# Optimization experiments

Measured on AMD Instinct MI355X. Metric: run time of the kernel, lower is better.

The kernel has to match this reference:

```python
import jax, jax.numpy as jnp
import numpy as np
from jax import lax

B, N, C = 8, 8192, 64
ODR, K, OUT = 4, 32, 128
S = N // ODR
EPS = 1e-5


def _lbr(h, W, b, g, be):
    # h: [M, K, Cin] -> linear -> BN (training-mode batch stats over (M,K) per channel) -> relu
    y = jnp.einsum('mki,oi->mko', h, W) + b
    mean = y.mean(axis=(0, 1))
    var = ((y - mean) ** 2).mean(axis=(0, 1))  # biased var, as torch BN uses for normalization
    y = (y - mean) * lax.rsqrt(var + EPS) * g + be
    return jax.nn.relu(y)


def setup_inputs() -> dict:
    key = jax.random.key(0)
    ks = jax.random.split(key, 12)
    x = jax.random.normal(ks[0], (B, N, C), dtype=jnp.float32)
    coor = jax.random.normal(ks[1], (B, N, 3), dtype=jnp.float32)
    indx = jax.random.permutation(ks[2], N)[:S]  # like torch.randperm(N)[:S]
    w1 = jax.random.normal(ks[3], (OUT, 2 * C), dtype=jnp.float32) * (2 * C) ** -0.5
    b1 = jax.random.normal(ks[4], (OUT,), dtype=jnp.float32) * 0.01
    g1 = jax.random.uniform(ks[5], (OUT,), dtype=jnp.float32, minval=0.5, maxval=1.5)
    be1 = jax.random.normal(ks[6], (OUT,), dtype=jnp.float32) * 0.01
    w2 = jax.random.normal(ks[7], (OUT, OUT), dtype=jnp.float32) * OUT ** -0.5
    b2 = jax.random.normal(ks[8], (OUT,), dtype=jnp.float32) * 0.01
    g2 = jax.random.uniform(ks[9], (OUT,), dtype=jnp.float32, minval=0.5, maxval=1.5)
    be2 = jax.random.normal(ks[10], (OUT,), dtype=jnp.float32) * 0.01
    return dict(x=x, coor=coor, indx=indx, w1=w1, b1=b1, g1=g1, be1=be1,
                w2=w2, b2=b2, g2=g2, be2=be2)


def reference(x, coor, indx, w1, b1, g1, be1, w2, b2, g2, be2):
    sampled_coor = coor[:, indx, :]  # [B,S,3]
    sampled_x = x[:, indx, :]        # [B,S,C]
    # pairwise squared distances [B,S,N]
    dist = jnp.sum((coor[:, None, :, :] - sampled_coor[:, :, None, :]) ** 2, axis=-1)
    # k smallest distances == argsort(dist)[..., :K]
    _, knn_idx = lax.top_k(-dist, K)  # [B,S,K]
    knn_x = jax.vmap(lambda xb, ib: xb[ib])(x, knn_idx)  # [B,S,K,C]
    rep_x = jnp.broadcast_to(sampled_x[:, :, None, :], (x.shape[0], S, K, x.shape[2]))
    feat = jnp.concatenate([rep_x, knn_x - rep_x], axis=-1)  # [B,S,K,2C]
    feat = feat.reshape(x.shape[0] * S, K, 2 * x.shape[2])
    h = _lbr(feat, w1, b1, g1, be1)
    h = _lbr(h, w2, b2, g2, be2)
    h = h.reshape(x.shape[0], S, K, -1)
    out = jnp.max(h, axis=2)  # [B,S,OUT]
    return out, sampled_coor
```

## Files before the change

### kernel.cpp

```cpp
#include <hip/hip_runtime.h>
#include <stdint.h>


#define N_    8192
#define GPB_  16

typedef __attribute__((ext_vector_type(8))) short bf8;
typedef __attribute__((ext_vector_type(16))) float f32x16;
typedef __attribute__((ext_vector_type(2))) float f32x2;

__device__ __forceinline__ unsigned int bf1u(float f) {
  unsigned int u = __float_as_uint(f);
  return (u + 0x7fffu + ((u >> 16) & 1u)) >> 16;
}
__device__ __forceinline__ unsigned int bfpair(float lo, float hi) {
  return bf1u(lo) | (bf1u(hi) << 16);
}

__device__ __forceinline__ f32x2 pk_add(f32x2 a, f32x2 b) {
  f32x2 d;
  asm("v_pk_add_f32 %0, %1, %2" : "=v"(d) : "v"(a), "v"(b));
  return d;
}
__device__ __forceinline__ f32x2 pk_mul(f32x2 a, f32x2 b) {
  f32x2 d;
  asm("v_pk_mul_f32 %0, %1, %2" : "=v"(d) : "v"(a), "v"(b));
  return d;
}

__global__ __launch_bounds__(256) void kprep(const float* __restrict__ w1,
                                             const float* __restrict__ w2,
                                             const float* __restrict__ coor,
                                             const int* __restrict__ indx,
                                             unsigned short* __restrict__ w1b,
                                             unsigned short* __restrict__ w2b,
                                             float* __restrict__ outc,
                                             float* __restrict__ soa) {
  int e = blockIdx.x * 256 + threadIdx.x;
  if (e < 16384) {
    w1b[e] = (unsigned short)bf1u(w1[e]);
  } else if (e < 32768) {
    int e2 = e - 16384;
    w2b[e2] = (unsigned short)bf1u(w2[e2]);
  } else if (e < 81920) {
    int e2 = e - 32768;
    int bs = e2 / 3, c = e2 - bs * 3;
    int b = bs >> 11, s = bs & 2047;
    outc[e2] = coor[(b * N_ + indx[s]) * 3 + c];
  } else {
    int p = e - 81920;
    const int b = p >> 13, i = p & 8191;
    const float* src = coor + (size_t)p * 3;
    float* dst = soa + b * 24576;
    dst[i]         = src[0];
    dst[8192 + i]  = src[1];
    dst[16384 + i] = src[2];
  }
}

__global__ __launch_bounds__(256, 8) void kknn(const float* __restrict__ soa,
                                               const int* __restrict__ indx,
                                               int* __restrict__ knn) {
  __shared__ __align__(16) float4 sdist4[4 * 256];
  __shared__ float sTw[8];
  __shared__ unsigned long long cands[192];
  __shared__ int ccnt;

  const int gid = blockIdx.x;
  const int b = gid >> 11, s = gid & 2047;
  const int tid = threadIdx.x;
  const int w = tid >> 6, lane = tid & 63;
  const int hl = lane & 31;
  const float* Xb = soa + b * 24576;
  const float* Yb = Xb + 8192;
  const float* Zb = Xb + 16384;
  const int qi = indx[s];
  const float qx = Xb[qi], qy = Yb[qi], qz = Zb[qi];
  const f32x2 nqx = {-qx, -qx}, nqy = {-qy, -qy}, nqz = {-qz, -qz};

  f32x2 rd[8];
  float dmA = 3.4e38f, dmB = 3.4e38f;
#pragma unroll
  for (int it = 0; it < 8; ++it) {
    const int ofs = (it << 10) + (tid << 2);
    union { float4 f4; f32x2 h[2]; } X, Y, Z;
    X.f4 = *(const float4*)(Xb + ofs);
    Y.f4 = *(const float4*)(Yb + ofs);
    Z.f4 = *(const float4*)(Zb + ofs);
    const f32x2 dxl = pk_add(X.h[0], nqx), dyl = pk_add(Y.h[0], nqy),
                dzl = pk_add(Z.h[0], nqz);
    const f32x2 dxh = pk_add(X.h[1], nqx), dyh = pk_add(Y.h[1], nqy),
                dzh = pk_add(Z.h[1], nqz);
    const f32x2 sl =
        pk_add(pk_add(pk_mul(dxl, dxl), pk_mul(dyl, dyl)), pk_mul(dzl, dzl));
    const f32x2 sh =
        pk_add(pk_add(pk_mul(dxh, dxh), pk_mul(dyh, dyh)), pk_mul(dzh, dzh));
    dmA = fminf(fminf(sl.x, sl.y), dmA);
    dmB = fminf(fminf(sh.x, sh.y), dmB);
    if (it < 4) {
      rd[it * 2] = sl;
      rd[it * 2 + 1] = sh;
    } else {
      union { float4 f4; f32x2 h[2]; } st;
      st.h[0] = sl;
      st.h[1] = sh;
      sdist4[((it - 4) << 8) + tid] = st.f4;
    }
  }
  float dmin = fminf(dmA, dmB);
  if (tid == 0) ccnt = 0;
  if (tid < 192) cands[tid] = ~0ULL;

  float v = dmin;
#pragma unroll
  for (int k = 2; k <= 32; k <<= 1) {
#pragma unroll
    for (int j = k >> 1; j >= 1; j >>= 1) {
      const float o = __shfl_xor(v, j, 64);
      const bool dirAsc = ((hl & k) == 0);
      const bool lower = ((hl & j) == 0);
      const float lo = fminf(v, o), hi = fmaxf(v, o);
      v = (dirAsc == lower) ? lo : hi;
    }
  }
  if (hl == 3) sTw[(w << 1) + (lane >> 5)] = v;
  __syncthreads();
  const float T =
      fmaxf(fmaxf(fmaxf(sTw[0], sTw[1]), fmaxf(sTw[2], sTw[3])),
            fmaxf(fmaxf(sTw[4], sTw[5]), fmaxf(sTw[6], sTw[7])));

#pragma unroll
  for (int t = 0; t < 8; ++t) {
    const int p0 = ((t >> 1) << 10) + (tid << 2) + ((t & 1) << 1);
    const float d0 = rd[t].x, d1 = rd[t].y;
    if (d0 <= T) {
      const int pos = atomicAdd(&ccnt, 1);
      if (pos < 192)
        cands[pos] = ((unsigned long long)__float_as_uint(d0) << 32) |
                     (unsigned int)p0;
    }
    if (d1 <= T) {
      const int pos = atomicAdd(&ccnt, 1);
      if (pos < 192)
        cands[pos] = ((unsigned long long)__float_as_uint(d1) << 32) |
                     (unsigned int)(p0 + 1);
    }
  }
#pragma unroll
  for (int it = 4; it < 8; ++it) {
    const float4 d4 = sdist4[((it - 4) << 8) + tid];
    const int p0 = (it << 10) + (tid << 2);
    const float dd[4] = {d4.x, d4.y, d4.z, d4.w};
#pragma unroll
    for (int j = 0; j < 4; ++j) {
      if (dd[j] <= T) {
        const int pos = atomicAdd(&ccnt, 1);
        if (pos < 192)
          cands[pos] = ((unsigned long long)__float_as_uint(dd[j]) << 32) |
                       (unsigned int)(p0 + j);
      }
    }
  }
  __syncthreads();

  const int E = min(ccnt, 192);
  if (tid < E) {
    const unsigned long long key = cands[tid];
    int rank = 0;
    const int Ep = (E + 3) & ~3;
#pragma unroll 4
    for (int j = 0; j < Ep; ++j) rank += (cands[j] < key) ? 1 : 0;
    if (rank < 32) knn[gid * 32 + rank] = (int)(unsigned int)key;
  }
}

template <int PHASE>
__global__ __launch_bounds__(256, 2) void kphase(
    const float* __restrict__ x, const int* __restrict__ indx,
    const int* __restrict__ knn, const float* __restrict__ b1,
    const unsigned short* __restrict__ w1b, const unsigned short* __restrict__ w2b,
    const float* __restrict__ b2, const float* __restrict__ st1,
    float* __restrict__ part, float* __restrict__ mout) {
  __shared__ __align__(16) unsigned short sxb[4][80];
  __shared__ __align__(16) unsigned short dls[4][32 * 68 + 8];
  __shared__ __align__(16) unsigned short h1[PHASE == 2 ? 2 * 32 * 136 : 8];

  const int tid = threadIdx.x;
  const int w = tid >> 6;
  const int lane = tid & 63;
  const int m = lane & 31, q2 = lane >> 5;
  const int col = (w << 5) + m;
  const int r8 = tid >> 3, c8 = (tid & 7) * 8;

  const int bb = blockIdx.x & 7;
  const int jj = blockIdx.x >> 3;
  const float* xb = x + (size_t)bb * (N_ * 64);
  const int gidbase = (bb << 11) + jj * GPB_;
  const int sbase = jj * GPB_;

  bf8 bf1[8];
#pragma unroll
  for (int t = 0; t < 8; ++t)
    bf1[t] = *(const bf8*)&w1b[col * 128 + t * 16 + q2 * 8];
  bf8 bf2[8];
  float s1 = 0.f, t1 = 0.f, b2v = 0.f;
  if constexpr (PHASE == 2) {
#pragma unroll
    for (int t = 0; t < 8; ++t)
      bf2[t] = *(const bf8*)&w2b[col * 128 + t * 16 + q2 * 8];
    s1 = st1[col];
    t1 = st1[128 + col];
    b2v = b2[col];
  }
  (void)w2b; (void)b2; (void)st1; (void)mout;
  const float b1c = b1[col];

  float sum = 0.f, ssq = 0.f;

  float4 caA, ccA, gaA, gcA, caB, ccB, gaB, gcB;
  {
    const int idxA = indx[sbase];
    const int idxB = indx[sbase + 1];
    const int nbrA = knn[(size_t)gidbase * 32 + r8];
    const int nbrB = knn[(size_t)(gidbase + 1) * 32 + r8];
    const float* cA = xb + (size_t)idxA * 64;
    caA = *(const float4*)(cA + c8);
    ccA = *(const float4*)(cA + c8 + 4);
    const float* gA = xb + (size_t)nbrA * 64;
    gaA = *(const float4*)(gA + c8);
    gcA = *(const float4*)(gA + c8 + 4);
    const float* cB = xb + (size_t)idxB * 64;
    caB = *(const float4*)(cB + c8);
    ccB = *(const float4*)(cB + c8 + 4);
    const float* gB = xb + (size_t)nbrB * 64;
    gaB = *(const float4*)(gB + c8);
    gcB = *(const float4*)(gB + c8 + 4);
  }
  int idxA2 = (GPB_ > 2) ? indx[sbase + 2] : 0;
  int idxB2 = (GPB_ > 3) ? indx[sbase + 3] : 0;
  int nbrA2 = (GPB_ > 2) ? knn[(size_t)(gidbase + 2) * 32 + r8] : 0;
  int nbrB2 = (GPB_ > 3) ? knn[(size_t)(gidbase + 3) * 32 + r8] : 0;

#pragma unroll 1
  for (int g = 0; g < GPB_; g += 2) {
    const int gid = gidbase + g;
    const int p0 = g & 3, p1 = (g + 1) & 3;

    float4 caA_n = caA, ccA_n = ccA, gaA_n = gaA, gcA_n = gcA;
    float4 caB_n = caB, ccB_n = ccB, gaB_n = gaB, gcB_n = gcB;
    if (g + 2 < GPB_) {
      const float* cA = xb + (size_t)idxA2 * 64;
      caA_n = *(const float4*)(cA + c8);
      ccA_n = *(const float4*)(cA + c8 + 4);
      const float* gA = xb + (size_t)nbrA2 * 64;
      gaA_n = *(const float4*)(gA + c8);
      gcA_n = *(const float4*)(gA + c8 + 4);
      const float* cB = xb + (size_t)idxB2 * 64;
      caB_n = *(const float4*)(cB + c8);
      ccB_n = *(const float4*)(cB + c8 + 4);
      const float* gB = xb + (size_t)nbrB2 * 64;
      gaB_n = *(const float4*)(gB + c8);
      gcB_n = *(const float4*)(gB + c8 + 4);
    }
    if (g + 4 < GPB_) {
      nbrA2 = knn[(size_t)(gid + 4) * 32 + r8];
      nbrB2 = knn[(size_t)(gid + 5) * 32 + r8];
      idxA2 = indx[sbase + g + 4];
      idxB2 = indx[sbase + g + 5];
    }

    {
      uint2 lo, hi;
      lo.x = bfpair(gaA.x - caA.x, gaA.y - caA.y);
      lo.y = bfpair(gaA.z - caA.z, gaA.w - caA.w);
      hi.x = bfpair(gcA.x - ccA.x, gcA.y - ccA.y);
      hi.y = bfpair(gcA.z - ccA.z, gcA.w - ccA.w);
      *(uint2*)&dls[p0][r8 * 68 + c8] = lo;
      *(uint2*)&dls[p0][r8 * 68 + c8 + 4] = hi;
      lo.x = bfpair(gaB.x - caB.x, gaB.y - caB.y);
      lo.y = bfpair(gaB.z - caB.z, gaB.w - caB.w);
      hi.x = bfpair(gcB.x - ccB.x, gcB.y - ccB.y);
      hi.y = bfpair(gcB.z - ccB.z, gcB.w - ccB.w);
      *(uint2*)&dls[p1][r8 * 68 + c8] = lo;
      *(uint2*)&dls[p1][r8 * 68 + c8 + 4] = hi;
    }
    if (tid < 8) {
      uint2 lo, hi;
      lo.x = bfpair(caA.x, caA.y);
      lo.y = bfpair(caA.z, caA.w);
      hi.x = bfpair(ccA.x, ccA.y);
      hi.y = bfpair(ccA.z, ccA.w);
      *(uint2*)&sxb[p0][tid * 8] = lo;
      *(uint2*)&sxb[p0][tid * 8 + 4] = hi;
      lo.x = bfpair(caB.x, caB.y);
      lo.y = bfpair(caB.z, caB.w);
      hi.x = bfpair(ccB.x, ccB.y);
      hi.y = bfpair(ccB.z, ccB.w);
      *(uint2*)&sxb[p1][tid * 8] = lo;
      *(uint2*)&sxb[p1][tid * 8 + 4] = hi;
    }
    asm volatile("s_waitcnt lgkmcnt(0)" ::: "memory");
    __builtin_amdgcn_s_barrier();

#pragma unroll
    for (int mem = 0; mem < 2; ++mem) {
      const int pb = mem == 0 ? p0 : p1;
      bf8 af[8];
#pragma unroll
      for (int t = 0; t < 4; ++t) {
        union { bf8 v; uint2 u[2]; } fa;
        fa.u[0] = *(const uint2*)&sxb[pb][t * 16 + q2 * 8];
        fa.u[1] = *(const uint2*)&sxb[pb][t * 16 + q2 * 8 + 4];
        af[t] = fa.v;
      }
#pragma unroll
      for (int t = 0; t < 4; ++t) {
        union { bf8 v; uint2 u[2]; } fa;
        fa.u[0] = *(const uint2*)&dls[pb][m * 68 + t * 16 + q2 * 8];
        fa.u[1] = *(const uint2*)&dls[pb][m * 68 + t * 16 + q2 * 8 + 4];
        af[4 + t] = fa.v;
      }
      f32x16 acc;
#pragma unroll
      for (int r = 0; r < 16; ++r) acc[r] = b1c;
#pragma unroll
      for (int t = 0; t < 8; ++t)
        acc = __builtin_amdgcn_mfma_f32_32x32x16_bf16(af[t], bf1[t], acc, 0, 0, 0);

      if constexpr (PHASE == 1) {
#pragma unroll
        for (int r = 0; r < 16; ++r) {
          const float v = acc[r];
          sum += v;
          ssq = fmaf(v, v, ssq);
        }
      } else {
        const int hp = mem * (32 * 136);
#pragma unroll
        for (int r = 0; r < 16; ++r) {
          const float hv = fmaxf(0.f, fmaf(acc[r], s1, t1));
          const int row = (r & 3) + ((r >> 2) << 3) + (q2 << 2);
          h1[hp + row * 136 + col] = (unsigned short)bf1u(hv);
        }
      }
    }

    if constexpr (PHASE == 2) {
      asm volatile("s_waitcnt lgkmcnt(0)" ::: "memory");
      __builtin_amdgcn_s_barrier();
#pragma unroll
      for (int mem = 0; mem < 2; ++mem) {
        const int hp = mem * (32 * 136);
        f32x16 acc2;
#pragma unroll
        for (int r = 0; r < 16; ++r) acc2[r] = b2v;
#pragma unroll
        for (int t = 0; t < 8; ++t) {
          const bf8 a2 = *(const bf8*)&h1[hp + m * 136 + t * 16 + q2 * 8];
          acc2 = __builtin_amdgcn_mfma_f32_32x32x16_bf16(a2, bf2[t], acc2, 0, 0, 0);
        }
        float mx = -1e30f;
#pragma unroll
        for (int r = 0; r < 16; ++r) {
          const float v = acc2[r];
          sum += v;
          ssq = fmaf(v, v, ssq);
          mx = fmaxf(mx, v);
        }
        mx = fmaxf(mx, __shfl_xor(mx, 32, 64));
        if (lane < 32) mout[(size_t)(gid + mem) * 128 + col] = mx;
      }
    }

    caA = caA_n; ccA = ccA_n; gaA = gaA_n; gcA = gcA_n;
    caB = caB_n; ccB = ccB_n; gaB = gaB_n; gcB = gcB_n;
  }

  sum += __shfl_xor(sum, 32, 64);
  ssq += __shfl_xor(ssq, 32, 64);
  if (lane < 32) {
    part[blockIdx.x * 256 + col] = sum;
    part[blockIdx.x * 256 + 128 + col] = ssq;
  }
}

__global__ __launch_bounds__(256) void kred1(const float* __restrict__ part,
                                             double* __restrict__ dbuf) {
  const int blk = blockIdx.x;
  const int c = threadIdx.x;
  const float* p = part + (size_t)blk * 16 * 256 + c;
  double acc = 0.0;
#pragma unroll
  for (int r = 0; r < 16; ++r) acc += (double)p[r * 256];
  dbuf[blk * 256 + c] = acc;
}

__global__ __launch_bounds__(256) void kred2(const double* __restrict__ dbuf,
                                             const float* __restrict__ gam,
                                             const float* __restrict__ bet,
                                             float* __restrict__ st) {
  __shared__ double sS[256];
  const int c = threadIdx.x;
  double acc = 0.0;
#pragma unroll 8
  for (int i = 0; i < 64; ++i) acc += dbuf[i * 256 + c];
  sS[c] = acc;
  __syncthreads();
  if (c < 128) {
    const double Sv = sS[c], SSv = sS[128 + c];
    const double cnt = 524288.0;
    const double mean = Sv / cnt;
    const double var = SSv / cnt - mean * mean;
    const double scale = (double)gam[c] / sqrt(var + 1e-5);
    st[c] = (float)scale;
    st[128 + c] = (float)((double)bet[c] - mean * scale);
  }
}

__global__ __launch_bounds__(256) void kout(const float* __restrict__ m,
                                            const float* __restrict__ st2,
                                            float* __restrict__ out) {
  const int e4 = blockIdx.x * 256 + threadIdx.x;
  const int o0 = (e4 & 31) * 4;
  const float4 v = ((const float4*)m)[e4];
  const float4 sc = *(const float4*)&st2[o0];
  const float4 sh = *(const float4*)&st2[128 + o0];
  float4 r;
  r.x = fmaxf(0.f, fmaf(v.x, sc.x, sh.x));
  r.y = fmaxf(0.f, fmaf(v.y, sc.y, sh.y));
  r.z = fmaxf(0.f, fmaf(v.z, sc.z, sh.z));
  r.w = fmaxf(0.f, fmaf(v.w, sc.w, sh.w));
  ((float4*)out)[e4] = r;
}

extern "C" void kernel_launch(void* const* d_in, const int* in_sizes, int n_in,
                              void* d_out, int out_size, void* d_ws, size_t ws_size,
                              hipStream_t stream) {
  (void)in_sizes; (void)n_in; (void)out_size; (void)ws_size;
  const float* x    = (const float*)d_in[0];
  const float* coor = (const float*)d_in[1];
  const int*   indx = (const int*)d_in[2];
  const float* w1   = (const float*)d_in[3];
  const float* b1   = (const float*)d_in[4];
  const float* g1   = (const float*)d_in[5];
  const float* be1  = (const float*)d_in[6];
  const float* w2   = (const float*)d_in[7];
  const float* b2   = (const float*)d_in[8];
  const float* g2   = (const float*)d_in[9];
  const float* be2  = (const float*)d_in[10];
  float* out = (float*)d_out;

  char* ws = (char*)d_ws;
  int*            knn   = (int*)(ws + 0);
  float*          mbuf  = (float*)(ws + 2097152);
  float*          part1 = (float*)(ws + 10485760);
  float*          soa   = (float*)(ws + 10485760);
  float*          part2 = (float*)(ws + 12582912);
  unsigned short* w1b   = (unsigned short*)(ws + 14680064);
  unsigned short* w2b   = (unsigned short*)(ws + 14712832);
  float*          st1   = (float*)(ws + 14745600);
  float*          st2   = (float*)(ws + 14746624);
  double*         dbuf  = (double*)(ws + 14747648);

  float* outc = out + 2097152;

  kprep<<<576, 256, 0, stream>>>(w1, w2, coor, indx, w1b, w2b, outc, soa);
  kknn<<<16384, 256, 0, stream>>>(soa, indx, knn);
  kphase<1><<<1024, 256, 0, stream>>>(x, indx, knn, b1, w1b, w2b, b2, nullptr,
                                      part1, nullptr);
  kred1<<<64, 256, 0, stream>>>(part1, dbuf);
  kred2<<<1, 256, 0, stream>>>(dbuf, g1, be1, st1);
  kphase<2><<<1024, 256, 0, stream>>>(x, indx, knn, b1, w1b, w2b, b2, st1,
                                      part2, mbuf);
  kred1<<<64, 256, 0, stream>>>(part2, dbuf);
  kred2<<<1, 256, 0, stream>>>(dbuf, g2, be2, st2);
  kout<<<2048, 256, 0, stream>>>(mbuf, st2, out);
}
```

Measured before the change: 243.4 us.

## Stage bf16 difference tiles in workspace during phase 1 for reuse in phase 2

```diff
diff --git a/kernel.cpp b/kernel.cpp
--- a/kernel.cpp
+++ b/kernel.cpp
@@ -4,6 +4,9 @@
 
 #define N_    8192
 #define GPB_  16
+#define TILE_OFF_  14878720ull
+#define SXB_OFF_   81987584ull
+#define WS_NEED_   84084736ull
 
 typedef __attribute__((ext_vector_type(8))) short bf8;
 typedef __attribute__((ext_vector_type(16))) float f32x16;
@@ -174,13 +177,14 @@
   }
 }
 
-template <int PHASE>
+template <int PHASE, int STAGED>
 __global__ __launch_bounds__(256, 2) void kphase(
     const float* __restrict__ x, const int* __restrict__ indx,
     const int* __restrict__ knn, const float* __restrict__ b1,
     const unsigned short* __restrict__ w1b, const unsigned short* __restrict__ w2b,
     const float* __restrict__ b2, const float* __restrict__ st1,
-    float* __restrict__ part, float* __restrict__ mout) {
+    float* __restrict__ part, float* __restrict__ mout,
+    uint4* __restrict__ tbuf, uint4* __restrict__ sbuf) {
   __shared__ __align__(16) unsigned short sxb[4][80];
   __shared__ __align__(16) unsigned short dls[4][32 * 68 + 8];
   __shared__ __align__(16) unsigned short h1[PHASE == 2 ? 2 * 32 * 136 : 8];
@@ -212,129 +216,72 @@
     t1 = st1[128 + col];
     b2v = b2[col];
   }
-  (void)w2b; (void)b2; (void)st1; (void)mout;
+  (void)w2b; (void)b2; (void)st1; (void)mout; (void)tbuf; (void)sbuf;
   const float b1c = b1[col];
 
   float sum = 0.f, ssq = 0.f;
 
-  float4 caA, ccA, gaA, gcA, caB, ccB, gaB, gcB;
-  {
-    const int idxA = indx[sbase];
-    const int idxB = indx[sbase + 1];
-    const int nbrA = knn[(size_t)gidbase * 32 + r8];
-    const int nbrB = knn[(size_t)(gidbase + 1) * 32 + r8];
-    const float* cA = xb + (size_t)idxA * 64;
-    caA = *(const float4*)(cA + c8);
-    ccA = *(const float4*)(cA + c8 + 4);
-    const float* gA = xb + (size_t)nbrA * 64;
-    gaA = *(const float4*)(gA + c8);
-    gcA = *(const float4*)(gA + c8 + 4);
-    const float* cB = xb + (size_t)idxB * 64;
-    caB = *(const float4*)(cB + c8);
-    ccB = *(const float4*)(cB + c8 + 4);
-    const float* gB = xb + (size_t)nbrB * 64;
-    gaB = *(const float4*)(gB + c8);
-    gcB = *(const float4*)(gB + c8 + 4);
-  }
-  int idxA2 = (GPB_ > 2) ? indx[sbase + 2] : 0;
-  int idxB2 = (GPB_ > 3) ? indx[sbase + 3] : 0;
-  int nbrA2 = (GPB_ > 2) ? knn[(size_t)(gidbase + 2) * 32 + r8] : 0;
-  int nbrB2 = (GPB_ > 3) ? knn[(size_t)(gidbase + 3) * 32 + r8] : 0;
+  if constexpr (PHASE == 2 && STAGED == 1) {
+    uint4 tA = tbuf[(size_t)gidbase * 256 + tid];
+    uint4 tB = tbuf[(size_t)(gidbase + 1) * 256 + tid];
+    uint4 sA, sB;
+    if (tid < 8) {
+      sA = sbuf[(size_t)gidbase * 8 + tid];
+      sB = sbuf[(size_t)(gidbase + 1) * 8 + tid];
+    }
 
 #pragma unroll 1
-  for (int g = 0; g < GPB_; g += 2) {
-    const int gid = gidbase + g;
-    const int p0 = g & 3, p1 = (g + 1) & 3;
-
-    float4 caA_n = caA, ccA_n = ccA, gaA_n = gaA, gcA_n = gcA;
-    float4 caB_n = caB, ccB_n = ccB, gaB_n = gaB, gcB_n = gcB;
-    if (g + 2 < GPB_) {
-      const float* cA = xb + (size_t)idxA2 * 64;
-      caA_n = *(const float4*)(cA + c8);
-      ccA_n = *(const float4*)(cA + c8 + 4);
-      const float* gA = xb + (size_t)nbrA2 * 64;
-      gaA_n = *(const float4*)(gA + c8);
-      gcA_n = *(const float4*)(gA + c8 + 4);
-      const float* cB = xb + (size_t)idxB2 * 64;
-      caB_n = *(const float4*)(cB + c8);
-      ccB_n = *(const float4*)(cB + c8 + 4);
-      const float* gB = xb + (size_t)nbrB2 * 64;
-      gaB_n = *(const float4*)(gB + c8);
-      gcB_n = *(const float4*)(gB + c8 + 4);
-    }
-    if (g + 4 < GPB_) {
-      nbrA2 = knn[(size_t)(gid + 4) * 32 + r8];
-      nbrB2 = knn[(size_t)(gid + 5) * 32 + r8];
-      idxA2 = indx[sbase + g + 4];
-      idxB2 = indx[sbase + g + 5];
-    }
-
-    {
-      uint2 lo, hi;
-      lo.x = bfpair(gaA.x - caA.x, gaA.y - caA.y);
-      lo.y = bfpair(gaA.z - caA.z, gaA.w - caA.w);
-      hi.x = bfpair(gcA.x - ccA.x, gcA.y - ccA.y);
-      hi.y = bfpair(gcA.z - ccA.z, gcA.w - ccA.w);
-      *(uint2*)&dls[p0][r8 * 68 + c8] = lo;
-      *(uint2*)&dls[p0][r8 * 68 + c8 + 4] = hi;
-      lo.x = bfpair(gaB.x - caB.x, gaB.y - caB.y);
-      lo.y = bfpair(gaB.z - caB.z, gaB.w - caB.w);
-      hi.x = bfpair(gcB.x - ccB.x, gcB.y - ccB.y);
-      hi.y = bfpair(gcB.z - ccB.z, gcB.w - ccB.w);
-      *(uint2*)&dls[p1][r8 * 68 + c8] = lo;
-      *(uint2*)&dls[p1][r8 * 68 + c8 + 4] = hi;
-    }
-    if (tid < 8) {
-      uint2 lo, hi;
-      lo.x = bfpair(caA.x, caA.y);
-      lo.y = bfpair(caA.z, caA.w);
-      hi.x = bfpair(ccA.x, ccA.y);
-      hi.y = bfpair(ccA.z, ccA.w);
-      *(uint2*)&sxb[p0][tid * 8] = lo;
-      *(uint2*)&sxb[p0][tid * 8 + 4] = hi;
-      lo.x = bfpair(caB.x, caB.y);
-      lo.y = bfpair(caB.z, caB.w);
-      hi.x = bfpair(ccB.x, ccB.y);
-      hi.y = bfpair(ccB.z, ccB.w);
-      *(uint2*)&sxb[p1][tid * 8] = lo;
-      *(uint2*)&sxb[p1][tid * 8 + 4] = hi;
-    }
-    asm volatile("s_waitcnt lgkmcnt(0)" ::: "memory");
-    __builtin_amdgcn_s_barrier();
-
-#pragma unroll
-    for (int mem = 0; mem < 2; ++mem) {
-      const int pb = mem == 0 ? p0 : p1;
-      bf8 af[8];
-#pragma unroll
-      for (int t = 0; t < 4; ++t) {
-        union { bf8 v; uint2 u[2]; } fa;
-        fa.u[0] = *(const uint2*)&sxb[pb][t * 16 + q2 * 8];
-        fa.u[1] = *(const uint2*)&sxb[pb][t * 16 + q2 * 8 + 4];
-        af[t] = fa.v;
-      }
-#pragma unroll
-      for (int t = 0; t < 4; ++t) {
-        union { bf8 v; uint2 u[2]; } fa;
-        fa.u[0] = *(const uint2*)&dls[pb][m * 68 + t * 16 + q2 * 8];
-        fa.u[1] = *(const uint2*)&dls[pb][m * 68 + t * 16 + q2 * 8 + 4];
-        af[4 + t] = fa.v;
-      }
-      f32x16 acc;
-#pragma unroll
-      for (int r = 0; r < 16; ++r) acc[r] = b1c;
-#pragma unroll
-      for (int t = 0; t < 8; ++t)
-        acc = __builtin_amdgcn_mfma_f32_32x32x16_bf16(af[t], bf1[t], acc, 0, 0, 0);
-
-      if constexpr (PHASE == 1) {
-#pragma unroll
-        for (int r = 0; r < 16; ++r) {
-          const float v = acc[r];
-          sum += v;
-          ssq = fmaf(v, v, ssq);
-        }
-      } else {
+    for (int g = 0; g < GPB_; g += 2) {
+      const int gid = gidbase + g;
+      const int p0 = g & 3, p1 = (g + 1) & 3;
+
+      uint4 tA_n = tA, tB_n = tB, sA_n = sA, sB_n = sB;
+      if (g + 2 < GPB_) {
+        tA_n = tbuf[(size_t)(gid + 2) * 256 + tid];
+        tB_n = tbuf[(size_t)(gid + 3) * 256 + tid];
+        if (tid < 8) {
+          sA_n = sbuf[(size_t)(gid + 2) * 8 + tid];
+          sB_n = sbuf[(size_t)(gid + 3) * 8 + tid];
+        }
+      }
+
+      *(uint2*)&dls[p0][r8 * 68 + c8] = make_uint2(tA.x, tA.y);
+      *(uint2*)&dls[p0][r8 * 68 + c8 + 4] = make_uint2(tA.z, tA.w);
+      *(uint2*)&dls[p1][r8 * 68 + c8] = make_uint2(tB.x, tB.y);
+      *(uint2*)&dls[p1][r8 * 68 + c8 + 4] = make_uint2(tB.z, tB.w);
+      if (tid < 8) {
+        *(uint2*)&sxb[p0][tid * 8] = make_uint2(sA.x, sA.y);
+        *(uint2*)&sxb[p0][tid * 8 + 4] = make_uint2(sA.z, sA.w);
+        *(uint2*)&sxb[p1][tid * 8] = make_uint2(sB.x, sB.y);
+        *(uint2*)&sxb[p1][tid * 8 + 4] = make_uint2(sB.z, sB.w);
+      }
+      asm volatile("s_waitcnt lgkmcnt(0)" ::: "memory");
+      __builtin_amdgcn_s_barrier();
+
+#pragma unroll
+      for (int mem = 0; mem < 2; ++mem) {
+        const int pb = mem == 0 ? p0 : p1;
+        bf8 af[8];
+#pragma unroll
+        for (int t = 0; t < 4; ++t) {
+          union { bf8 v; uint2 u[2]; } fa;
+          fa.u[0] = *(const uint2*)&sxb[pb][t * 16 + q2 * 8];
+          fa.u[1] = *(const uint2*)&sxb[pb][t * 16 + q2 * 8 + 4];
+          af[t] = fa.v;
+        }
+#pragma unroll
+        for (int t = 0; t < 4; ++t) {
+          union { bf8 v; uint2 u[2]; } fa;
+          fa.u[0] = *(const uint2*)&dls[pb][m * 68 + t * 16 + q2 * 8];
+          fa.u[1] = *(const uint2*)&dls[pb][m * 68 + t * 16 + q2 * 8 + 4];
+          af[4 + t] = fa.v;
+        }
+        f32x16 acc;
+#pragma unroll
+        for (int r = 0; r < 16; ++r) acc[r] = b1c;
+#pragma unroll
+        for (int t = 0; t < 8; ++t)
+          acc = __builtin_amdgcn_mfma_f32_32x32x16_bf16(af[t], bf1[t], acc, 0, 0, 0);
         const int hp = mem * (32 * 136);
 #pragma unroll
         for (int r = 0; r < 16; ++r) {
@@ -343,9 +290,7 @@
           h1[hp + row * 136 + col] = (unsigned short)bf1u(hv);
         }
       }
-    }
-
-    if constexpr (PHASE == 2) {
+
       asm volatile("s_waitcnt lgkmcnt(0)" ::: "memory");
       __builtin_amdgcn_s_barrier();
 #pragma unroll
@@ -370,10 +315,176 @@
         mx = fmaxf(mx, __shfl_xor(mx, 32, 64));
         if (lane < 32) mout[(size_t)(gid + mem) * 128 + col] = mx;
       }
-    }
-
-    caA = caA_n; ccA = ccA_n; gaA = gaA_n; gcA = gcA_n;
-    caB = caB_n; ccB = ccB_n; gaB = gaB_n; gcB = gcB_n;
+
+      tA = tA_n; tB = tB_n; sA = sA_n; sB = sB_n;
+    }
+  } else {
+    float4 caA, ccA, gaA, gcA, caB, ccB, gaB, gcB;
+    {
+      const int idxA = indx[sbase];
+      const int idxB = indx[sbase + 1];
+      const int nbrA = knn[(size_t)gidbase * 32 + r8];
+      const int nbrB = knn[(size_t)(gidbase + 1) * 32 + r8];
+      const float* cA = xb + (size_t)idxA * 64;
+      caA = *(const float4*)(cA + c8);
+      ccA = *(const float4*)(cA + c8 + 4);
+      const float* gA = xb + (size_t)nbrA * 64;
+      gaA = *(const float4*)(gA + c8);
+      gcA = *(const float4*)(gA + c8 + 4);
+      const float* cB = xb + (size_t)idxB * 64;
+      caB = *(const float4*)(cB + c8);
+      ccB = *(const float4*)(cB + c8 + 4);
+      const float* gB = xb + (size_t)nbrB * 64;
+      gaB = *(const float4*)(gB + c8);
+      gcB = *(const float4*)(gB + c8 + 4);
+    }
+    int idxA2 = (GPB_ > 2) ? indx[sbase + 2] : 0;
+    int idxB2 = (GPB_ > 3) ? indx[sbase + 3] : 0;
+    int nbrA2 = (GPB_ > 2) ? knn[(size_t)(gidbase + 2) * 32 + r8] : 0;
+    int nbrB2 = (GPB_ > 3) ? knn[(size_t)(gidbase + 3) * 32 + r8] : 0;
+
+#pragma unroll 1
+    for (int g = 0; g < GPB_; g += 2) {
+      const int gid = gidbase + g;
+      const int p0 = g & 3, p1 = (g + 1) & 3;
+
+      float4 caA_n = caA, ccA_n = ccA, gaA_n = gaA, gcA_n = gcA;
+      float4 caB_n = caB, ccB_n = ccB, gaB_n = gaB, gcB_n = gcB;
+      if (g + 2 < GPB_) {
+        const float* cA = xb + (size_t)idxA2 * 64;
+        caA_n = *(const float4*)(cA + c8);
+        ccA_n = *(const float4*)(cA + c8 + 4);
+        const float* gA = xb + (size_t)nbrA2 * 64;
+        gaA_n = *(const float4*)(gA + c8);
+        gcA_n = *(const float4*)(gA + c8 + 4);
+        const float* cB = xb + (size_t)idxB2 * 64;
+        caB_n = *(const float4*)(cB + c8);
+        ccB_n = *(const float4*)(cB + c8 + 4);
+        const float* gB = xb + (size_t)nbrB2 * 64;
+        gaB_n = *(const float4*)(gB + c8);
+        gcB_n = *(const float4*)(gB + c8 + 4);
+      }
+      if (g + 4 < GPB_) {
+        nbrA2 = knn[(size_t)(gid + 4) * 32 + r8];
+        nbrB2 = knn[(size_t)(gid + 5) * 32 + r8];
+        idxA2 = indx[sbase + g + 4];
+        idxB2 = indx[sbase + g + 5];
+      }
+
+      {
+        uint2 lo, hi;
+        lo.x = bfpair(gaA.x - caA.x, gaA.y - caA.y);
+        lo.y = bfpair(gaA.z - caA.z, gaA.w - caA.w);
+        hi.x = bfpair(gcA.x - ccA.x, gcA.y - ccA.y);
+        hi.y = bfpair(gcA.z - ccA.z, gcA.w - ccA.w);
+        *(uint2*)&dls[p0][r8 * 68 + c8] = lo;
+        *(uint2*)&dls[p0][r8 * 68 + c8 + 4] = hi;
+        if constexpr (PHASE == 1 && STAGED == 1)
+          tbuf[(size_t)gid * 256 + tid] = make_uint4(lo.x, lo.y, hi.x, hi.y);
+        lo.x = bfpair(gaB.x - caB.x, gaB.y - caB.y);
+        lo.y = bfpair(gaB.z - caB.z, gaB.w - caB.w);
+        hi.x = bfpair(gcB.x - ccB.x, gcB.y - ccB.y);
+        hi.y = bfpair(gcB.z - ccB.z, gcB.w - ccB.w);
+        *(uint2*)&dls[p1][r8 * 68 + c8] = lo;
+        *(uint2*)&dls[p1][r8 * 68 + c8 + 4] = hi;
+        if constexpr (PHASE == 1 && STAGED == 1)
+          tbuf[(size_t)(gid + 1) * 256 + tid] = make_uint4(lo.x, lo.y, hi.x, hi.y);
+      }
+      if (tid < 8) {
+        uint2 lo, hi;
+        lo.x = bfpair(caA.x, caA.y);
+        lo.y = bfpair(caA.z, caA.w);
+        hi.x = bfpair(ccA.x, ccA.y);
+        hi.y = bfpair(ccA.z, ccA.w);
+        *(uint2*)&sxb[p0][tid * 8] = lo;
+        *(uint2*)&sxb[p0][tid * 8 + 4] = hi;
+        if constexpr (PHASE == 1 && STAGED == 1)
+          sbuf[(size_t)gid * 8 + tid] = make_uint4(lo.x, lo.y, hi.x, hi.y);
+        lo.x = bfpair(caB.x, caB.y);
+        lo.y = bfpair(caB.z, caB.w);
+        hi.x = bfpair(ccB.x, ccB.y);
+        hi.y = bfpair(ccB.z, ccB.w);
+        *(uint2*)&sxb[p1][tid * 8] = lo;
+        *(uint2*)&sxb[p1][tid * 8 + 4] = hi;
+        if constexpr (PHASE == 1 && STAGED == 1)
+          sbuf[(size_t)(gid + 1) * 8 + tid] = make_uint4(lo.x, lo.y, hi.x, hi.y);
+      }
+      asm volatile("s_waitcnt lgkmcnt(0)" ::: "memory");
+      __builtin_amdgcn_s_barrier();
+
+#pragma unroll
+      for (int mem = 0; mem < 2; ++mem) {
+        const int pb = mem == 0 ? p0 : p1;
+        bf8 af[8];
+#pragma unroll
+        for (int t = 0; t < 4; ++t) {
+          union { bf8 v; uint2 u[2]; } fa;
+          fa.u[0] = *(const uint2*)&sxb[pb][t * 16 + q2 * 8];
+          fa.u[1] = *(const uint2*)&sxb[pb][t * 16 + q2 * 8 + 4];
+          af[t] = fa.v;
+        }
+#pragma unroll
+        for (int t = 0; t < 4; ++t) {
+          union { bf8 v; uint2 u[2]; } fa;
+          fa.u[0] = *(const uint2*)&dls[pb][m * 68 + t * 16 + q2 * 8];
+          fa.u[1] = *(const uint2*)&dls[pb][m * 68 + t * 16 + q2 * 8 + 4];
+          af[4 + t] = fa.v;
+        }
+        f32x16 acc;
+#pragma unroll
+        for (int r = 0; r < 16; ++r) acc[r] = b1c;
+#pragma unroll
+        for (int t = 0; t < 8; ++t)
+          acc = __builtin_amdgcn_mfma_f32_32x32x16_bf16(af[t], bf1[t], acc, 0, 0, 0);
+
+        if constexpr (PHASE == 1) {
+#pragma unroll
+          for (int r = 0; r < 16; ++r) {
+            const float v = acc[r];
+            sum += v;
+            ssq = fmaf(v, v, ssq);
+          }
+        } else {
+          const int hp = mem * (32 * 136);
+#pragma unroll
+          for (int r = 0; r < 16; ++r) {
+            const float hv = fmaxf(0.f, fmaf(acc[r], s1, t1));
+            const int row = (r & 3) + ((r >> 2) << 3) + (q2 << 2);
+            h1[hp + row * 136 + col] = (unsigned short)bf1u(hv);
+          }
+        }
+      }
+
+      if constexpr (PHASE == 2) {
+        asm volatile("s_waitcnt lgkmcnt(0)" ::: "memory");
+        __builtin_amdgcn_s_barrier();
+#pragma unroll
+        for (int mem = 0; mem < 2; ++mem) {
+          const int hp = mem * (32 * 136);
+          f32x16 acc2;
+#pragma unroll
+          for (int r = 0; r < 16; ++r) acc2[r] = b2v;
+#pragma unroll
+          for (int t = 0; t < 8; ++t) {
+            const bf8 a2 = *(const bf8*)&h1[hp + m * 136 + t * 16 + q2 * 8];
+            acc2 = __builtin_amdgcn_mfma_f32_32x32x16_bf16(a2, bf2[t], acc2, 0, 0, 0);
+          }
+          float mx = -1e30f;
+#pragma unroll
+          for (int r = 0; r < 16; ++r) {
+            const float v = acc2[r];
+            sum += v;
+            ssq = fmaf(v, v, ssq);
+            mx = fmaxf(mx, v);
+          }
+          mx = fmaxf(mx, __shfl_xor(mx, 32, 64));
+          if (lane < 32) mout[(size_t)(gid + mem) * 128 + col] = mx;
+        }
+      }
+
+      caA = caA_n; ccA = ccA_n; gaA = gaA_n; gcA = gcA_n;
+      caB = caB_n; ccB = ccB_n; gaB = gaB_n; gcB = gcB_n;
+    }
   }
 
   sum += __shfl_xor(sum, 32, 64);
@@ -436,7 +547,7 @@
 extern "C" void kernel_launch(void* const* d_in, const int* in_sizes, int n_in,
                               void* d_out, int out_size, void* d_ws, size_t ws_size,
                               hipStream_t stream) {
-  (void)in_sizes; (void)n_in; (void)out_size; (void)ws_size;
+  (void)in_sizes; (void)n_in; (void)out_size;
   const float* x    = (const float*)d_in[0];
   const float* coor = (const float*)d_in[1];
   const int*   indx = (const int*)d_in[2];
@@ -461,17 +572,29 @@
   float*          st1   = (float*)(ws + 14745600);
   float*          st2   = (float*)(ws + 14746624);
   double*         dbuf  = (double*)(ws + 14747648);
+  uint4*          tbuf  = (uint4*)(ws + TILE_OFF_);
+  uint4*          sbuf  = (uint4*)(ws + SXB_OFF_);
 
   float* outc = out + 2097152;
+  const bool useTiles = (ws_size >= WS_NEED_);
 
   kprep<<<576, 256, 0, stream>>>(w1, w2, coor, indx, w1b, w2b, outc, soa);
   kknn<<<16384, 256, 0, stream>>>(soa, indx, knn);
-  kphase<1><<<1024, 256, 0, stream>>>(x, indx, knn, b1, w1b, w2b, b2, nullptr,
-                                      part1, nullptr);
-  kred1<<<64, 256, 0, stream>>>(part1, dbuf);
-  kred2<<<1, 256, 0, stream>>>(dbuf, g1, be1, st1);
-  kphase<2><<<1024, 256, 0, stream>>>(x, indx, knn, b1, w1b, w2b, b2, st1,
-                                      part2, mbuf);
+  if (useTiles) {
+    kphase<1, 1><<<1024, 256, 0, stream>>>(x, indx, knn, b1, w1b, w2b, b2,
+                                           nullptr, part1, nullptr, tbuf, sbuf);
+    kred1<<<64, 256, 0, stream>>>(part1, dbuf);
+    kred2<<<1, 256, 0, stream>>>(dbuf, g1, be1, st1);
+    kphase<2, 1><<<1024, 256, 0, stream>>>(x, indx, knn, b1, w1b, w2b, b2, st1,
+                                           part2, mbuf, tbuf, sbuf);
+  } else {
+    kphase<1, 0><<<1024, 256, 0, stream>>>(x, indx, knn, b1, w1b, w2b, b2,
+                                           nullptr, part1, nullptr, tbuf, sbuf);
+    kred1<<<64, 256, 0, stream>>>(part1, dbuf);
+    kred2<<<1, 256, 0, stream>>>(dbuf, g1, be1, st1);
+    kphase<2, 0><<<1024, 256, 0, stream>>>(x, indx, knn, b1, w1b, w2b, b2, st1,
+                                           part2, mbuf, tbuf, sbuf);
+  }
   kred1<<<64, 256, 0, stream>>>(part2, dbuf);
   kred2<<<1, 256, 0, stream>>>(dbuf, g2, be2, st2);
   kout<<<2048, 256, 0, stream>>>(mbuf, st2, out);
```

Result: slower. 251.0 us (+3.1%).
